# Performance work log

Measured on AMD Instinct MI355X. Metric: run time of the kernel, lower is better.

## Reference

```python
import jax, jax.numpy as jnp
import numpy as np

DIM = 1024
NUM_PATTERNS = 8192
B, S = 2, 4096


def setup_inputs() -> dict:
    key = jax.random.key(0)
    k1, k2, k3 = jax.random.split(key, 3)
    scale = 1.0 / np.sqrt(DIM)
    x = jax.random.normal(k1, (B, S, DIM), dtype=jnp.float32)
    # nn.Linear default init ~ U(-1/sqrt(in), 1/sqrt(in)); normal*scale is fine for a baseline
    w_q = jax.random.normal(k2, (DIM, DIM), dtype=jnp.float32) * scale
    xi = jax.random.normal(k3, (NUM_PATTERNS, DIM), dtype=jnp.float32) * scale
    beta = jnp.float32(1.0 / np.sqrt(DIM))
    return {"x": x, "w_q": w_q, "xi": xi, "beta": beta}


def reference(x, w_q, xi, beta):
    # q = x @ w_q.T  (torch F.linear convention: weight is [out, in])
    q = jnp.einsum("bsd,ed->bse", x, w_q)
    # logits = beta * q @ xi.T  -> [B, S, P]
    logits = beta * jnp.einsum("bsd,pd->bsp", q, xi)
    attn = jax.nn.softmax(logits, axis=-1)
    # retrieve patterns: attn @ xi -> [B, S, dim]
    return jnp.einsum("bsp,pd->bsd", attn, xi)
```

## Files before the change

kernel.cpp:

```cpp
#include <hip/hip_runtime.h>


typedef __attribute__((ext_vector_type(8))) int int8v;
typedef __attribute__((ext_vector_type(4))) float f32x4;

#define NDIM 1024
#define NPAT 8192
#define NROW 8192

__device__ __forceinline__ unsigned f8pack4(float a, float b, float c, float d) {
  int w = __builtin_amdgcn_cvt_pk_fp8_f32(a, b, 0, false);
  w = __builtin_amdgcn_cvt_pk_fp8_f32(c, d, w, true);
  return (unsigned)w;
}
__device__ __forceinline__ unsigned char f8b(float v) {
  return (unsigned char)(__builtin_amdgcn_cvt_pk_fp8_f32(v, v, 0, false) & 0xff);
}
__device__ __forceinline__ int sig(int c) {
  return (c & 64) | ((c & 15) << 2) | ((c >> 4) & 3);
}

__device__ __forceinline__ void gload_lds16(const void* g, void* l) {
  __builtin_amdgcn_global_load_lds(
      (const __attribute__((address_space(1))) unsigned char*)g,
      (__attribute__((address_space(3))) unsigned char*)l,
      16, 0, 0);
}


__global__ void cast_f8(const float* __restrict__ in,
                        unsigned* __restrict__ out, float scale, int n4) {
  int i = blockIdx.x * blockDim.x + threadIdx.x;
  if (i < n4) {
    float4 v = ((const float4*)in)[i];
    out[i] = f8pack4(v.x * scale, v.y * scale, v.z * scale, v.w * scale);
  }
}

__global__ void xi_prep8(const float* __restrict__ xi,
                         unsigned char* __restrict__ xi8,
                         unsigned char* __restrict__ xit8,
                         float* __restrict__ colsum) {
  __shared__ float t[32][33];
  __shared__ float cs[8][32];
  int tx = threadIdx.x, ty = threadIdx.y;
  int d0 = blockIdx.x * 32, p0 = blockIdx.y * 32;
  int d = d0 + tx;
  int di = (d & ~127) + sig(d & 127);
  float psum = 0.f;
#pragma unroll
  for (int j = 0; j < 32; j += 8) {
    float v = xi[(long)(p0 + ty + j) * NDIM + d];
    t[ty + j][tx] = v;
    psum += v;
    xi8[(long)(p0 + ty + j) * NDIM + di] = f8b(32.f * v);
  }
  cs[ty][tx] = psum;
  __syncthreads();
  if (ty == 0) {
    float s = 0.f;
#pragma unroll
    for (int k = 0; k < 8; ++k) s += cs[k][tx];
    atomicAdd(&colsum[d0 + tx], s);
  }
  int p = p0 + tx;
  int pi = (p & ~127) + sig(p & 127);
#pragma unroll
  for (int j = 0; j < 32; j += 8)
    xit8[(long)(d0 + ty + j) * NPAT + pi] = f8b(32.f * t[tx][ty + j]);
}


template <int MODE>
__launch_bounds__(256, 2)
__global__ void gemm_f8(const unsigned char* __restrict__ A,
                        const unsigned char* __restrict__ B,
                        void* __restrict__ Cv, int N, int K,
                        const float* __restrict__ beta_ptr,
                        const float* __restrict__ rowsum,
                        const float* __restrict__ colsum,
                        float* __restrict__ rowsum_out) {
  __shared__ unsigned char smem[65536];

  const int tid = threadIdx.x;
  const int wave = tid >> 6;
  const int lane = tid & 63;
  const int wm = wave >> 1, wn = wave & 1;
  const int quad = lane >> 4, ln = lane & 15;

  const long row0 = (long)blockIdx.y * 128;
  const long col0 = (long)blockIdx.x * 128;

  const int r_in = lane >> 3;
  const int csl = lane & 7;
  const int cg = ((((csl >> 1) ^ (r_in & 3)) << 1) | (csl & 1));
  const unsigned char* gA[4];
  const unsigned char* gB[4];
  int lA[4], lB[4];
#pragma unroll
  for (int p = 0; p < 4; ++p) {
    int grp = wave * 4 + p;
    gA[p] = A + (row0 + grp * 8 + r_in) * (long)K + cg * 16;
    gB[p] = B + (col0 + grp * 8 + r_in) * (long)K + cg * 16;
    lA[p] = grp * 1024;
    lB[p] = 16384 + grp * 1024;
  }

  const int ps = (quad ^ (ln & 3)) * 32;
  const int base_a = (wm * 64 + ln) * 128 + ps;
  const int base_b = 16384 + (wn * 64 + ln) * 128 + ps;

  f32x4 acc[4][4] = {};
  const int nkt = K >> 7;

#pragma unroll
  for (int p = 0; p < 4; ++p) gload_lds16(gA[p], smem + lA[p]);
#pragma unroll
  for (int p = 0; p < 4; ++p) gload_lds16(gB[p], smem + lB[p]);
#pragma unroll
  for (int p = 0; p < 4; ++p) { gA[p] += 128; gB[p] += 128; }
  __syncthreads();

#pragma unroll 2
  for (int kt = 0; kt < nkt; ++kt) {
    const unsigned char* sb = smem + (kt & 1) * 32768;
    unsigned char* sn = smem + ((kt + 1) & 1) * 32768;

    if (kt + 1 < nkt) {
#pragma unroll
      for (int p = 0; p < 4; ++p) gload_lds16(gA[p], sn + lA[p]);
#pragma unroll
      for (int p = 0; p < 4; ++p) gload_lds16(gB[p], sn + lB[p]);
#pragma unroll
      for (int p = 0; p < 4; ++p) { gA[p] += 128; gB[p] += 128; }
    }

    int8v af[4], bfv[4];
#pragma unroll
    for (int t = 0; t < 4; ++t)
      af[t] = *(const int8v*)(sb + base_a + t * 2048);
#pragma unroll
    for (int t = 0; t < 4; ++t)
      bfv[t] = *(const int8v*)(sb + base_b + t * 2048);
    __builtin_amdgcn_s_setprio(1);
#pragma unroll
    for (int mt = 0; mt < 4; ++mt)
#pragma unroll
      for (int nt = 0; nt < 4; ++nt)
        acc[mt][nt] = __builtin_amdgcn_mfma_scale_f32_16x16x128_f8f6f4(
            af[mt], bfv[nt], acc[mt][nt], 0, 0, 0, 0x7f7f7f7f, 0, 0x7f7f7f7f);
    __builtin_amdgcn_s_setprio(0);

    __syncthreads();
  }

  if (MODE == 0) {
    unsigned* C32 = (unsigned*)Cv;
    const float s = 1.0f / 32.0f;
#pragma unroll
    for (int mt = 0; mt < 4; ++mt)
#pragma unroll
      for (int r = 0; r < 4; ++r) {
        long row = row0 + wm * 64 + mt * 16 + quad * 4 + r;
        unsigned w = f8pack4(acc[mt][0][r] * s, acc[mt][1][r] * s,
                             acc[mt][2][r] * s, acc[mt][3][r] * s);
        C32[row * (N >> 2) + (col0 >> 2) + wn * 16 + ln] = w;
      }
  } else if (MODE == 1) {
    unsigned* C32 = (unsigned*)Cv;
    const float bs = beta_ptr[0] * (1.0f / 32.0f);
#pragma unroll
    for (int mt = 0; mt < 4; ++mt)
#pragma unroll
      for (int r = 0; r < 4; ++r) {
        long row = row0 + wm * 64 + mt * 16 + quad * 4 + r;
        float e0 = (__expf(bs * acc[mt][0][r]) - 1.0f) * 32.f;
        float e1 = (__expf(bs * acc[mt][1][r]) - 1.0f) * 32.f;
        float e2 = (__expf(bs * acc[mt][2][r]) - 1.0f) * 32.f;
        float e3 = (__expf(bs * acc[mt][3][r]) - 1.0f) * 32.f;
        C32[row * (N >> 2) + (col0 >> 2) + wn * 16 + ln] =
            f8pack4(e0, e1, e2, e3);
        float s = e0 + e1 + e2 + e3;
        s += __shfl_xor(s, 1, 64);
        s += __shfl_xor(s, 2, 64);
        s += __shfl_xor(s, 4, 64);
        s += __shfl_xor(s, 8, 64);
        if (ln == 0) atomicAdd(&rowsum_out[row], s);
      }
  } else {
    float* C = (float*)Cv;
#pragma unroll
    for (int mt = 0; mt < 4; ++mt)
#pragma unroll
      for (int r = 0; r < 4; ++r) {
        long row = row0 + wm * 64 + mt * 16 + quad * 4 + r;
        float inv = 1.0f / (8192.0f + rowsum[row] * (1.0f / 32.0f));
#pragma unroll
        for (int nt = 0; nt < 4; ++nt) {
          long col = col0 + wn * 64 + nt * 16 + ln;
          C[row * N + col] =
              (acc[mt][nt][r] * (1.0f / 1024.0f) + colsum[col]) * inv;
        }
      }
  }
}


extern "C" void kernel_launch(void* const* d_in, const int* in_sizes, int n_in,
                              void* d_out, int out_size, void* d_ws,
                              size_t ws_size, hipStream_t stream) {
  const float* x    = (const float*)d_in[0];
  const float* wq   = (const float*)d_in[1];
  const float* xi   = (const float*)d_in[2];
  const float* beta = (const float*)d_in[3];
  float* out = (float*)d_out;

  char* ws = (char*)d_ws;
  const size_t MB = 1024 * 1024;
  unsigned char* x8   = (unsigned char*)(ws);
  unsigned char* wq8  = (unsigned char*)(ws + 8 * MB);
  unsigned char* q8   = (unsigned char*)(ws + 9 * MB);
  unsigned char* xi8  = (unsigned char*)(ws + 17 * MB);
  unsigned char* xit8 = (unsigned char*)(ws + 25 * MB);
  float*         rs   = (float*)(ws + 33 * MB);
  float*         csum = (float*)(ws + 33 * MB + 32768);
  unsigned char* E8   = (unsigned char*)(ws + 34 * MB);

  hipMemsetAsync(rs, 0, 36864, stream);

  cast_f8<<<(NROW * NDIM / 4) / 256, 256, 0, stream>>>(
      x, (unsigned*)x8, 1.0f, NROW * NDIM / 4);
  cast_f8<<<(NDIM * NDIM / 4) / 256, 256, 0, stream>>>(
      wq, (unsigned*)wq8, 32.0f, NDIM * NDIM / 4);
  xi_prep8<<<dim3(NDIM / 32, NPAT / 32), dim3(32, 8), 0, stream>>>(
      xi, xi8, xit8, csum);

  gemm_f8<0><<<dim3(NDIM / 128, NROW / 128), 256, 0, stream>>>(
      x8, wq8, q8, NDIM, NDIM, nullptr, nullptr, nullptr, nullptr);

  gemm_f8<1><<<dim3(NPAT / 128, NROW / 128), 256, 0, stream>>>(
      q8, xi8, E8, NPAT, NDIM, beta, nullptr, nullptr, rs);

  gemm_f8<2><<<dim3(NDIM / 128, NROW / 128), 256, 0, stream>>>(
      E8, xit8, out, NDIM, NPAT, nullptr, rs, csum, nullptr);
}
```

Baseline: 360.5 us.

## Enlarge FP8 GEMM tiles to 512 threads with phased load/MFMA interleaving

```diff
diff --git a/kernel.cpp b/kernel.cpp
--- a/kernel.cpp
+++ b/kernel.cpp
@@ -71,113 +71,151 @@
 }
 
 
-template <int MODE>
-__launch_bounds__(256, 2)
-__global__ void gemm_f8(const unsigned char* __restrict__ A,
-                        const unsigned char* __restrict__ B,
-                        void* __restrict__ Cv, int N, int K,
-                        const float* __restrict__ beta_ptr,
-                        const float* __restrict__ rowsum,
-                        const float* __restrict__ colsum,
-                        float* __restrict__ rowsum_out) {
-  __shared__ unsigned char smem[65536];
+#define CLUSTER(P)                                                          \
+  __builtin_amdgcn_s_setprio(1);                                            \
+  _Pragma("unroll") for (int mt = 0; mt < AP; ++mt)                         \
+    _Pragma("unroll") for (int nt = 0; nt < 4; ++nt)                        \
+      acc[(P) * AP + mt][nt] =                                              \
+          __builtin_amdgcn_mfma_scale_f32_16x16x128_f8f6f4(                 \
+              af[mt], bf[nt], acc[(P) * AP + mt][nt], 0, 0, 0, 0x7f7f7f7f,  \
+              0, 0x7f7f7f7f);                                               \
+  __builtin_amdgcn_s_setprio(0);
+
+template <int MODE, int BM>
+__launch_bounds__(512, 2)
+__global__ void gemm8(const unsigned char* __restrict__ A,
+                      const unsigned char* __restrict__ B,
+                      void* __restrict__ Cv, int N, int K,
+                      const float* __restrict__ beta_ptr,
+                      const float* __restrict__ rowsum,
+                      const float* __restrict__ colsum,
+                      float* __restrict__ rowsum_out) {
+  constexpr int MF = BM / 32;
+  constexpr int AP = MF / 4;
+  constexpr int AL = BM / 64;
+  constexpr int ABYTES = BM * 128;
+  constexpr int BUF = ABYTES + 32768;
+
+  __shared__ __attribute__((aligned(16))) unsigned char smem[2 * BUF];
 
   const int tid = threadIdx.x;
   const int wave = tid >> 6;
   const int lane = tid & 63;
-  const int wm = wave >> 1, wn = wave & 1;
+  const int wm = wave >> 2, wn = wave & 3;
   const int quad = lane >> 4, ln = lane & 15;
 
-  const long row0 = (long)blockIdx.y * 128;
-  const long col0 = (long)blockIdx.x * 128;
+  const int nbx = N >> 8;
+  const long row0 = (long)(blockIdx.x / nbx) * BM;
+  const long col0 = (long)(blockIdx.x % nbx) * 256;
+  const int nkt = K >> 7;
 
   const int r_in = lane >> 3;
   const int csl = lane & 7;
   const int cg = ((((csl >> 1) ^ (r_in & 3)) << 1) | (csl & 1));
-  const unsigned char* gA[4];
-  const unsigned char* gB[4];
-  int lA[4], lB[4];
-#pragma unroll
-  for (int p = 0; p < 4; ++p) {
-    int grp = wave * 4 + p;
-    gA[p] = A + (row0 + grp * 8 + r_in) * (long)K + cg * 16;
-    gB[p] = B + (col0 + grp * 8 + r_in) * (long)K + cg * 16;
-    lA[p] = grp * 1024;
-    lB[p] = 16384 + grp * 1024;
+  const unsigned char* pA[AL];
+  const unsigned char* pB[4];
+  int dA[AL], dB[4];
+#pragma unroll
+  for (int R = 0; R < AL; ++R) {
+    pA[R] = A + (row0 + wave * (BM / 8) + R * 8 + r_in) * (long)K + cg * 16;
+    dA[R] = (wave * (BM / 8) + R * 8) * 128;
+  }
+#pragma unroll
+  for (int R = 0; R < 4; ++R) {
+    pB[R] = B + (col0 + wave * 32 + R * 8 + r_in) * (long)K + cg * 16;
+    dB[R] = ABYTES + (wave * 32 + R * 8) * 128;
   }
 
   const int ps = (quad ^ (ln & 3)) * 32;
-  const int base_a = (wm * 64 + ln) * 128 + ps;
-  const int base_b = 16384 + (wn * 64 + ln) * 128 + ps;
-
-  f32x4 acc[4][4] = {};
-  const int nkt = K >> 7;
-
-#pragma unroll
-  for (int p = 0; p < 4; ++p) gload_lds16(gA[p], smem + lA[p]);
-#pragma unroll
-  for (int p = 0; p < 4; ++p) gload_lds16(gB[p], smem + lB[p]);
-#pragma unroll
-  for (int p = 0; p < 4; ++p) { gA[p] += 128; gB[p] += 128; }
-  __syncthreads();
+  const int bA = (wm * (BM / 2) + ln) * 128 + ps;
+  const int bB = ABYTES + (wn * 64 + ln) * 128 + ps;
+
+  f32x4 acc[MF][4] = {};
+
+#pragma unroll
+  for (int R = 0; R < AL; ++R) gload_lds16(pA[R], smem + dA[R]);
+#pragma unroll
+  for (int R = 0; R < 4; ++R) gload_lds16(pB[R], smem + dB[R]);
+#pragma unroll
+  for (int R = 0; R < AL; ++R) gload_lds16(pA[R] + 128, smem + BUF + dA[R]);
+  asm volatile("s_waitcnt vmcnt(%0)" ::"n"(AL) : "memory");
+  __builtin_amdgcn_s_barrier();
+  __builtin_amdgcn_sched_barrier(0);
 
 #pragma unroll 2
-  for (int kt = 0; kt < nkt; ++kt) {
-    const unsigned char* sb = smem + (kt & 1) * 32768;
-    unsigned char* sn = smem + ((kt + 1) & 1) * 32768;
-
-    if (kt + 1 < nkt) {
-#pragma unroll
-      for (int p = 0; p < 4; ++p) gload_lds16(gA[p], sn + lA[p]);
-#pragma unroll
-      for (int p = 0; p < 4; ++p) gload_lds16(gB[p], sn + lB[p]);
-#pragma unroll
-      for (int p = 0; p < 4; ++p) { gA[p] += 128; gB[p] += 128; }
-    }
-
-    int8v af[4], bfv[4];
-#pragma unroll
-    for (int t = 0; t < 4; ++t)
-      af[t] = *(const int8v*)(sb + base_a + t * 2048);
-#pragma unroll
-    for (int t = 0; t < 4; ++t)
-      bfv[t] = *(const int8v*)(sb + base_b + t * 2048);
-    __builtin_amdgcn_s_setprio(1);
-#pragma unroll
-    for (int mt = 0; mt < 4; ++mt)
-#pragma unroll
-      for (int nt = 0; nt < 4; ++nt)
-        acc[mt][nt] = __builtin_amdgcn_mfma_scale_f32_16x16x128_f8f6f4(
-            af[mt], bfv[nt], acc[mt][nt], 0, 0, 0, 0x7f7f7f7f, 0, 0x7f7f7f7f);
-    __builtin_amdgcn_s_setprio(0);
-
-    __syncthreads();
-  }
+  for (int i = 0; i < nkt; ++i) {
+    const int bo = (i & 1) * BUF;
+    const int nbo = BUF - bo;
+    const long o1 = (long)(i + 1 < nkt ? i + 1 : nkt - 1) << 7;
+    const long o2 = (long)(i + 2 < nkt ? i + 2 : nkt - 1) << 7;
+    int8v bf[4], af[AP];
+
+    gload_lds16(pB[0] + o1, smem + nbo + dB[0]);
+    gload_lds16(pB[1] + o1, smem + nbo + dB[1]);
+#pragma unroll
+    for (int nt = 0; nt < 4; ++nt)
+      bf[nt] = *(const int8v*)(smem + bo + bB + nt * 2048);
+#pragma unroll
+    for (int t = 0; t < AP; ++t)
+      af[t] = *(const int8v*)(smem + bo + bA + t * 2048);
+    CLUSTER(0)
+    __builtin_amdgcn_s_barrier();
+
+    gload_lds16(pB[2] + o1, smem + nbo + dB[2]);
+    gload_lds16(pB[3] + o1, smem + nbo + dB[3]);
+#pragma unroll
+    for (int t = 0; t < AP; ++t)
+      af[t] = *(const int8v*)(smem + bo + bA + (AP + t) * 2048);
+    CLUSTER(1)
+    __builtin_amdgcn_s_barrier();
+
+#pragma unroll
+    for (int t = 0; t < AP; ++t)
+      af[t] = *(const int8v*)(smem + bo + bA + (2 * AP + t) * 2048);
+    CLUSTER(2)
+    __builtin_amdgcn_s_barrier();
+
+#pragma unroll
+    for (int t = 0; t < AP; ++t)
+      af[t] = *(const int8v*)(smem + bo + bA + (3 * AP + t) * 2048);
+    asm volatile("s_waitcnt lgkmcnt(0)" ::: "memory");
+    __builtin_amdgcn_sched_barrier(0);
+    __builtin_amdgcn_s_barrier();
+    __builtin_amdgcn_sched_barrier(0);
+#pragma unroll
+    for (int R = 0; R < AL; ++R)
+      gload_lds16(pA[R] + o2, smem + bo + dA[R]);
+    CLUSTER(3)
+    asm volatile("s_waitcnt vmcnt(%0)" ::"n"(AL) : "memory");
+    __builtin_amdgcn_s_barrier();
+    __builtin_amdgcn_sched_barrier(0);
+  }
+  asm volatile("s_waitcnt vmcnt(0)" ::: "memory");
 
   if (MODE == 0) {
     unsigned* C32 = (unsigned*)Cv;
     const float s = 1.0f / 32.0f;
 #pragma unroll
-    for (int mt = 0; mt < 4; ++mt)
+    for (int mf = 0; mf < MF; ++mf)
 #pragma unroll
       for (int r = 0; r < 4; ++r) {
-        long row = row0 + wm * 64 + mt * 16 + quad * 4 + r;
-        unsigned w = f8pack4(acc[mt][0][r] * s, acc[mt][1][r] * s,
-                             acc[mt][2][r] * s, acc[mt][3][r] * s);
+        long row = row0 + wm * (BM / 2) + mf * 16 + quad * 4 + r;
+        unsigned w = f8pack4(acc[mf][0][r] * s, acc[mf][1][r] * s,
+                             acc[mf][2][r] * s, acc[mf][3][r] * s);
         C32[row * (N >> 2) + (col0 >> 2) + wn * 16 + ln] = w;
       }
   } else if (MODE == 1) {
     unsigned* C32 = (unsigned*)Cv;
     const float bs = beta_ptr[0] * (1.0f / 32.0f);
 #pragma unroll
-    for (int mt = 0; mt < 4; ++mt)
+    for (int mf = 0; mf < MF; ++mf)
 #pragma unroll
       for (int r = 0; r < 4; ++r) {
-        long row = row0 + wm * 64 + mt * 16 + quad * 4 + r;
-        float e0 = (__expf(bs * acc[mt][0][r]) - 1.0f) * 32.f;
-        float e1 = (__expf(bs * acc[mt][1][r]) - 1.0f) * 32.f;
-        float e2 = (__expf(bs * acc[mt][2][r]) - 1.0f) * 32.f;
-        float e3 = (__expf(bs * acc[mt][3][r]) - 1.0f) * 32.f;
+        long row = row0 + wm * (BM / 2) + mf * 16 + quad * 4 + r;
+        float e0 = (__expf(bs * acc[mf][0][r]) - 1.0f) * 32.f;
+        float e1 = (__expf(bs * acc[mf][1][r]) - 1.0f) * 32.f;
+        float e2 = (__expf(bs * acc[mf][2][r]) - 1.0f) * 32.f;
+        float e3 = (__expf(bs * acc[mf][3][r]) - 1.0f) * 32.f;
         C32[row * (N >> 2) + (col0 >> 2) + wn * 16 + ln] =
             f8pack4(e0, e1, e2, e3);
         float s = e0 + e1 + e2 + e3;
@@ -190,16 +228,16 @@
   } else {
     float* C = (float*)Cv;
 #pragma unroll
-    for (int mt = 0; mt < 4; ++mt)
+    for (int mf = 0; mf < MF; ++mf)
 #pragma unroll
       for (int r = 0; r < 4; ++r) {
-        long row = row0 + wm * 64 + mt * 16 + quad * 4 + r;
+        long row = row0 + wm * (BM / 2) + mf * 16 + quad * 4 + r;
         float inv = 1.0f / (8192.0f + rowsum[row] * (1.0f / 32.0f));
 #pragma unroll
         for (int nt = 0; nt < 4; ++nt) {
           long col = col0 + wn * 64 + nt * 16 + ln;
           C[row * N + col] =
-              (acc[mt][nt][r] * (1.0f / 1024.0f) + colsum[col]) * inv;
+              (acc[mf][nt][r] * (1.0f / 1024.0f) + colsum[col]) * inv;
         }
       }
   }
@@ -235,12 +273,12 @@
   xi_prep8<<<dim3(NDIM / 32, NPAT / 32), dim3(32, 8), 0, stream>>>(
       xi, xi8, xit8, csum);
 
-  gemm_f8<0><<<dim3(NDIM / 128, NROW / 128), 256, 0, stream>>>(
+  gemm8<0, 128><<<(NROW / 128) * (NDIM / 256), 512, 0, stream>>>(
       x8, wq8, q8, NDIM, NDIM, nullptr, nullptr, nullptr, nullptr);
 
-  gemm_f8<1><<<dim3(NPAT / 128, NROW / 128), 256, 0, stream>>>(
+  gemm8<1, 256><<<(NROW / 256) * (NPAT / 256), 512, 0, stream>>>(
       q8, xi8, E8, NPAT, NDIM, beta, nullptr, nullptr, rs);
 
-  gemm_f8<2><<<dim3(NDIM / 128, NROW / 128), 256, 0, stream>>>(
+  gemm8<2, 128><<<(NROW / 128) * (NDIM / 256), 512, 0, stream>>>(
       E8, xit8, out, NDIM, NPAT, nullptr, rs, csum, nullptr);
 }
```

Result: slower. 424.7 us (+17.8%).
